# Kernel optimization log

Hardware: AMD Instinct MI355X
Metric: run time of the kernel (lower is better)

Reference implementation:

```python
import jax, jax.numpy as jnp
import numpy as np

GROUP = 32  # hadamard_group_size == MXFP4 block size
FP4_GRID = np.array([0.0, 0.5, 1.0, 1.5, 2.0, 3.0, 4.0, 6.0], dtype=np.float32)  # e2m1 magnitudes
FP4_MID = np.array([0.25, 0.75, 1.25, 1.75, 2.5, 3.5, 5.0], dtype=np.float32)    # RTN midpoints


def _hadamard(n):
    # Sylvester construction, normalized so H is orthonormal (matches hadamard(n)*n**-0.5)
    H = np.array([[1.0]], dtype=np.float64)
    while H.shape[0] < n:
        H = np.block([[H, H], [H, -H]])
    return (H / np.sqrt(n)).astype(np.float32)


def _pseudo_quant_mxfp4(t, H, gs):
    """Hadamard-rotate per group of 32, then MXFP4 (e2m1 + power-of-two block scale)
    quant-dequant with abs_max scaling and a global scale. STE through the rounding."""
    shp = t.shape
    rot = t.reshape(-1, GROUP) @ H                      # [n_groups, 32] rotated space
    v = jax.lax.stop_gradient(rot) * gs
    absmax = jnp.max(jnp.abs(v), axis=-1, keepdims=True)
    # E8M0 power-of-two shared scale so that absmax/scale <= 6 (max e2m1 value)
    scale = jnp.exp2(jnp.ceil(jnp.log2(absmax / 6.0 + 1e-30)))
    scale = jnp.where(absmax > 0, scale, 1.0)
    u = v / scale
    grid = jnp.asarray(FP4_GRID)
    mid = jnp.asarray(FP4_MID)
    q = jnp.sign(u) * grid[jnp.searchsorted(mid, jnp.abs(u))]  # round-to-nearest e2m1
    dq = q * scale / gs
    out = rot + jax.lax.stop_gradient(dq - rot)         # straight-through estimator
    return out.reshape(shp)


def setup_inputs() -> dict:
    key = jax.random.key(0)
    kx, kw, kb = jax.random.split(key, 3)
    B, S, K, N = 4, 2048, 4096, 4096
    x = jax.random.normal(kx, (B, S, K), jnp.float32)
    weight = jax.random.normal(kw, (N, K), jnp.float32) * (K ** -0.5)
    bias = jax.random.normal(kb, (N,), jnp.float32)
    H = jnp.asarray(_hadamard(GROUP))
    weight_global_scale = jnp.array([3.0], jnp.float32)  # abs_max method
    act_global_scale = jnp.array([3.0], jnp.float32)
    return {"x": x, "weight": weight, "bias": bias, "hadamard_matrix": H,
            "weight_global_scale": weight_global_scale, "act_global_scale": act_global_scale}


def reference(x, weight, bias, hadamard_matrix, weight_global_scale, act_global_scale):
    x_dq = _pseudo_quant_mxfp4(x, hadamard_matrix, act_global_scale[0])
    w_dq = _pseudo_quant_mxfp4(weight, hadamard_matrix, weight_global_scale[0])
    # both operands stay in the rotated space; per-group Hadamard is orthogonal so
    # x_rot @ w_rot^T == x @ w^T up to quantization error (QuTLASS semantics)
    return jnp.einsum('bsk,nk->bsn', x_dq, w_dq) + bias
```

## Files before the change

kernel.cpp:

```cpp
#include <hip/hip_runtime.h>
#include <hip/hip_bf16.h>

typedef int   i32x4  __attribute__((ext_vector_type(4)));
typedef int   i32x8  __attribute__((ext_vector_type(8)));
typedef float f32x16 __attribute__((ext_vector_type(16)));

__device__ inline void gload_lds16(const void* g, void* l) {
  __builtin_amdgcn_global_load_lds((const __attribute__((address_space(1))) void*)g,
                                   (__attribute__((address_space(3))) void*)l, 16, 0, 0);
}
__device__ inline void gload_lds4(const void* g, void* l) {
  __builtin_amdgcn_global_load_lds((const __attribute__((address_space(1))) void*)g,
                                   (__attribute__((address_space(3))) void*)l, 4, 0, 0);
}
__device__ inline i32x8 pad8(i32x4 v) {
  i32x8 r;
  r[0] = v[0]; r[1] = v[1]; r[2] = v[2]; r[3] = v[3];
  r[4] = 0; r[5] = 0; r[6] = 0; r[7] = 0;
  return r;
}

__global__ __launch_bounds__(256) void quant_fused(const float* __restrict__ x,
                                                   const float* __restrict__ wt,
                                                   unsigned char* __restrict__ xq,
                                                   unsigned char* __restrict__ xsc,
                                                   unsigned char* __restrict__ wq,
                                                   unsigned char* __restrict__ wsc,
                                                   const float* __restrict__ ags,
                                                   const float* __restrict__ wgs,
                                                   int xg, int Mrows, int Nrows, int kg) {
  const int first = blockIdx.x * 256;
  const bool isX = first < xg;
  const float* in        = isX ? x   : wt;
  unsigned char* outq    = isX ? xq  : wq;
  unsigned char* outsc   = isX ? xsc : wsc;
  const float gs         = isX ? ags[0] : wgs[0];
  const int rows         = isX ? Mrows : Nrows;
  const int base         = isX ? first : first - xg;
  const int g = base + threadIdx.x;
  const int r = g / kg, j = g - r * kg;

  float t[32];
  const float4* p4 = (const float4*)(in + (size_t)g * 32);
#pragma unroll
  for (int i = 0; i < 8; ++i) {
    float4 v4 = p4[i];
    t[4 * i + 0] = v4.x; t[4 * i + 1] = v4.y;
    t[4 * i + 2] = v4.z; t[4 * i + 3] = v4.w;
  }
#pragma unroll
  for (int s = 0; s < 5; ++s) {
    const int hh = 1 << s;
#pragma unroll
    for (int i = 0; i < 32; ++i) {
      if ((i & hh) == 0) {
        float a = t[i], b = t[i + hh];
        t[i] = a + b;
        t[i + hh] = a - b;
      }
    }
  }

  const float c = 0.17677669529663687f;
  float v[32];
  float am = 0.0f;
#pragma unroll
  for (int i = 0; i < 32; ++i) {
    float vi = (t[i] * c) * gs;
    v[i] = vi;
    am = fmaxf(am, fabsf(vi));
  }

  float a6 = am / 6.0f;
  int ex;
  float mant = frexpf(a6, &ex);
  int e = (mant == 0.5f) ? ex - 1 : ex;
  if (e < -127) e = -127;
  if (e > 127) e = 127;
  float inv_s = ldexpf(1.0f, -e);

  unsigned int dw[4] = {0u, 0u, 0u, 0u};
#pragma unroll
  for (int i = 0; i < 32; ++i) {
    float u = v[i] * inv_s;
    float au = fabsf(u);
    int idx = (au > 0.25f) + (au > 0.75f) + (au > 1.25f) + (au > 1.75f)
            + (au > 2.5f) + (au > 3.5f) + (au > 5.0f);
    int code = idx | ((u < 0.0f) ? 8 : 0);
    dw[i >> 3] |= (unsigned)code << ((i & 7) * 4);
  }
  i32x4 packed;
  packed[0] = (int)dw[0]; packed[1] = (int)dw[1];
  packed[2] = (int)dw[2]; packed[3] = (int)dw[3];
  *(i32x4*)(outq + (size_t)r * ((size_t)kg * 16) + (size_t)j * 16) = packed;

  int s = j >> 3, j0 = j & 7;
  int p = ((j0 & 1) << 2) | (j0 >> 1);
  if (kg == 128) {
    __shared__ unsigned char sl[256];
    sl[(s << 4) | ((r & 1) << 3) | p] = (unsigned char)(e + 127);
    __syncthreads();
    if (threadIdx.x < 64) {
      int si = threadIdx.x >> 2, wd = threadIdx.x & 3;
      unsigned int vv = *(const unsigned int*)&sl[(si << 4) | (wd << 2)];
      size_t r0 = (size_t)(base / 128);
      *(unsigned int*)(outsc + ((size_t)si * rows + r0) * 8 + (wd << 2)) = vv;
    }
  } else {
    outsc[((size_t)s * rows + r) * 8 + p] = (unsigned char)(e + 127);
  }
}


#define STAGE(mb, kt, hh, ldsHalf) do {                                              \
    const unsigned char* _s = (mb) + (size_t)((hh)*64 + (w << 3) + (l >> 3)) * KB2   \
                      + (size_t)(kt) * 128 + (size_t)csw * 16;                       \
    gload_lds16(_s, (unsigned char*)(ldsHalf) + (w << 10));                          \
    gload_lds16(_s + ((size_t)KB2 << 5), (unsigned char*)(ldsHalf) + (w << 10) + 4096); \
  } while (0)

#define STAGE_ASC(kt, bf) gload_lds4(AscG + ((size_t)(kt) * M + brow) * 8 + (tid << 2), \
                                     (unsigned char*)&asc[bf][0] + (w << 8))
#define STAGE_BSC(kt, bf) gload_lds4(BscG + ((size_t)(kt) * N + bcol) * 8 + (tid << 2), \
                                     (unsigned char*)&bsc[bf][0] + (w << 8))

#define STAGESET(kt, bf) do {                                                        \
    STAGE(Bb, kt, 0, &lds[bf][1][0]); STAGE(Bb, kt, 1, &lds[bf][1][8192]);           \
    STAGE_BSC(kt, bf);                                                               \
    STAGE(Ab, kt, 0, &lds[bf][0][0]); STAGE(Ab, kt, 1, &lds[bf][0][8192]);           \
    STAGE_ASC(kt, bf);                                                               \
  } while (0)

#define LOADB(bf) do {                                                               \
    const unsigned char* _bb = &lds[bf][1][0];                                       \
    _Pragma("unroll")                                                                \
    for (int nt = 0; nt < 2; ++nt) {                                                 \
      int row = wn * 64 + nt * 32 + (l & 31);                                        \
      int xr = row & 7;                                                              \
      _Pragma("unroll")                                                              \
      for (int kk = 0; kk < 4; ++kk)                                                 \
        bfr[nt][kk] = *(const i32x4*)(_bb + row * 128 + (((kk * 2 + h) ^ xr) << 4)); \
      sb[nt] = *(const int*)((const unsigned char*)&bsc[bf][0] + row * 8 + h * 4);   \
    } } while (0)

#define LOADA(bf) do {                                                               \
    const unsigned char* _ab = &lds[bf][0][0];                                       \
    _Pragma("unroll")                                                                \
    for (int mt = 0; mt < 2; ++mt) {                                                 \
      int row = wm * 64 + mt * 32 + (l & 31);                                        \
      int xr = row & 7;                                                              \
      _Pragma("unroll")                                                              \
      for (int kk = 0; kk < 4; ++kk)                                                 \
        af[mt][kk] = *(const i32x4*)(_ab + row * 128 + (((kk * 2 + h) ^ xr) << 4));  \
      sa[mt] = *(const int*)((const unsigned char*)&asc[bf][0] + row * 8 + h * 4);   \
    } } while (0)

#define MF1(mt, nt, kk)                                                              \
  acc[mt][nt] = __builtin_amdgcn_mfma_scale_f32_32x32x64_f8f6f4(                     \
      pad8(af[mt][kk]), pad8(bfr[nt][kk]), acc[mt][nt], 4, 4, kk, sa[mt], kk, sb[nt]);

#define MFMAQ16() do {                                                               \
    __builtin_amdgcn_s_setprio(1);                                                   \
    MF1(0, 0, 0) MF1(0, 1, 0) MF1(1, 0, 0) MF1(1, 1, 0)                              \
    MF1(0, 0, 1) MF1(0, 1, 1) MF1(1, 0, 1) MF1(1, 1, 1)                              \
    MF1(0, 0, 2) MF1(0, 1, 2) MF1(1, 0, 2) MF1(1, 1, 2)                              \
    MF1(0, 0, 3) MF1(0, 1, 3) MF1(1, 0, 3) MF1(1, 1, 3)                              \
    __builtin_amdgcn_s_setprio(0);                                                   \
  } while (0)

#define DRAIN_THEN_BAR() do {                                                        \
    asm volatile("s_waitcnt lgkmcnt(0)" ::: "memory");                               \
    __builtin_amdgcn_sched_barrier(0);                                               \
    __builtin_amdgcn_s_barrier();                                                    \
  } while (0)

#define ENDP() __builtin_amdgcn_s_barrier()
#define VM10() asm volatile("s_waitcnt vmcnt(10)" ::: "memory")

__global__ __launch_bounds__(256, 2) void gemm128_fp4(const unsigned char* __restrict__ Aq,
                                                      const unsigned char* __restrict__ Bq,
                                                      const unsigned char* __restrict__ AscG,
                                                      const unsigned char* __restrict__ BscG,
                                                      float* __restrict__ C,
                                                      const float* __restrict__ bias,
                                                      const float* __restrict__ gsx,
                                                      const float* __restrict__ gsw,
                                                      int M, int N, int K) {
  __shared__ __align__(16) unsigned char lds[2][2][16384];
  __shared__ __align__(16) unsigned char asc[2][1024];
  __shared__ __align__(16) unsigned char bsc[2][1024];

  const int tid = threadIdx.x;
  const int w = tid >> 6, l = tid & 63;
  const int wm = w >> 1, wn = w & 1;
  const int h = l >> 5;
  const int csw = (l & 7) ^ (l >> 3);
  const int KB2 = K >> 1;

  const int ntn = N >> 7;
  const int nwg = gridDim.x;
  int r_t, c_t;
  {
    int bid = blockIdx.x;
    if ((nwg & 7) == 0) {
      int x = bid & 7, o = bid >> 3, cpx = nwg >> 3;
      int rpx = cpx / ntn;
      if ((ntn & 7) == 0 && rpx > 0 && (cpx % ntn) == 0) {
        int g8 = o & 7, rr = (o >> 3) % rpx, ss = o / (8 * rpx);
        r_t = x * rpx + rr;
        c_t = ss * 8 + g8;
      } else {
        int lin = x * cpx + o;
        r_t = lin / ntn; c_t = lin % ntn;
      }
    } else {
      r_t = bid / ntn; c_t = bid % ntn;
    }
  }
  const size_t brow = (size_t)r_t * 128;
  const size_t bcol = (size_t)c_t * 128;

  const unsigned char* Ab = Aq + brow * (size_t)KB2;
  const unsigned char* Bb = Bq + bcol * (size_t)KB2;

  f32x16 acc[2][2];
#pragma unroll
  for (int m = 0; m < 2; ++m)
#pragma unroll
    for (int n = 0; n < 2; ++n)
#pragma unroll
      for (int r = 0; r < 16; ++r) acc[m][n][r] = 0.0f;

  i32x4 af[2][4], bfr[2][4];
  int sa[2], sb[2];

  const int nkt = K / 256;

  STAGESET(0, 0);
  STAGESET(1, 1);
  VM10();
  __builtin_amdgcn_s_barrier();

  for (int t = 0; t < nkt; ++t) {
    const int p = t & 1;
    const int t2 = (t + 2 < nkt) ? t + 2 : nkt - 1;

    LOADB(p); LOADA(p);
    DRAIN_THEN_BAR();
    STAGESET(t2, p);
    __builtin_amdgcn_sched_barrier(0);
    MFMAQ16();
    VM10();
    ENDP();
  }

  const float inv = 1.0f / (gsx[0] * gsw[0]);
#pragma unroll
  for (int nt = 0; nt < 2; ++nt) {
    const int col = (int)bcol + wn * 64 + nt * 32 + (l & 31);
    const float bv = bias[col];
#pragma unroll
    for (int mt = 0; mt < 2; ++mt) {
      const size_t rbase = brow + (size_t)(wm * 64 + mt * 32 + 4 * h);
#pragma unroll
      for (int r = 0; r < 16; ++r) {
        const size_t row = rbase + (r & 3) + 8 * (r >> 2);
        C[row * (size_t)N + col] = acc[mt][nt][r] * inv + bv;
      }
    }
  }
}

extern "C" void kernel_launch(void* const* d_in, const int* in_sizes, int n_in,
                              void* d_out, int out_size, void* d_ws, size_t ws_size,
                              hipStream_t stream) {
  const float* x    = (const float*)d_in[0];
  const float* wgt  = (const float*)d_in[1];
  const float* bias = (const float*)d_in[2];
  const float* wgs  = (const float*)d_in[4];
  const float* ags  = (const float*)d_in[5];

  const int N = in_sizes[2];
  const int K = in_sizes[1] / N;
  const int M = in_sizes[0] / K;
  const int kg = K / 32;

  unsigned char* aq  = (unsigned char*)d_ws;
  unsigned char* bq  = aq + (size_t)M * (K / 2);
  unsigned char* asc = bq + (size_t)N * (K / 2);
  unsigned char* bsc = asc + (size_t)M * kg;

  const int xg = in_sizes[0] / 32;
  const int wg = in_sizes[1] / 32;
  quant_fused<<<dim3((xg + wg) / 256), dim3(256), 0, stream>>>(
      x, wgt, aq, asc, bq, bsc, ags, wgs, xg, M, N, kg);

  dim3 grid((M / 128) * (N / 128));
  gemm128_fp4<<<grid, dim3(256), 0, stream>>>(aq, bq, asc, bsc, (float*)d_out, bias,
                                              ags, wgs, M, N, K);
}
```

Measured before the change: 148.7 us.

## Split 128x128 FP4 GEMM tile across eight waves instead of four

Doubles the GEMM workgroup to 512 threads, arranged as a 2x4 grid of waves. Each wave now computes a 64x32 sub-tile (two MFMA accumulators instead of four), and the global-to-LDS staging loads are spread across the eight waves. The goal is more waves in flight to hide latency and fewer accumulator registers per wave. In exchange, A fragments are re-read from LDS by more waves, each wave has fewer MFMAs per barrier, and there is more barrier synchronization per unit of work.

```diff
diff --git a/kernel.cpp b/kernel.cpp
--- a/kernel.cpp
+++ b/kernel.cpp
@@ -112,36 +112,32 @@
 }
 
 
-#define STAGE(mb, kt, hh, ldsHalf) do {                                              \
+#define STAGE1(mb, kt, hh, ldsAB) do {                                               \
     const unsigned char* _s = (mb) + (size_t)((hh)*64 + (w << 3) + (l >> 3)) * KB2   \
                       + (size_t)(kt) * 128 + (size_t)csw * 16;                       \
-    gload_lds16(_s, (unsigned char*)(ldsHalf) + (w << 10));                          \
-    gload_lds16(_s + ((size_t)KB2 << 5), (unsigned char*)(ldsHalf) + (w << 10) + 4096); \
-  } while (0)
-
-#define STAGE_ASC(kt, bf) gload_lds4(AscG + ((size_t)(kt) * M + brow) * 8 + (tid << 2), \
-                                     (unsigned char*)&asc[bf][0] + (w << 8))
-#define STAGE_BSC(kt, bf) gload_lds4(BscG + ((size_t)(kt) * N + bcol) * 8 + (tid << 2), \
-                                     (unsigned char*)&bsc[bf][0] + (w << 8))
+    gload_lds16(_s, (unsigned char*)(ldsAB) + (hh) * 8192 + (w << 10));              \
+  } while (0)
 
 #define STAGESET(kt, bf) do {                                                        \
-    STAGE(Bb, kt, 0, &lds[bf][1][0]); STAGE(Bb, kt, 1, &lds[bf][1][8192]);           \
-    STAGE_BSC(kt, bf);                                                               \
-    STAGE(Ab, kt, 0, &lds[bf][0][0]); STAGE(Ab, kt, 1, &lds[bf][0][8192]);           \
-    STAGE_ASC(kt, bf);                                                               \
+    STAGE1(Bb, kt, 0, &lds[bf][1][0]); STAGE1(Bb, kt, 1, &lds[bf][1][0]);            \
+    STAGE1(Ab, kt, 0, &lds[bf][0][0]); STAGE1(Ab, kt, 1, &lds[bf][0][0]);            \
+    if (w < 4)                                                                       \
+      gload_lds4(AscG + ((size_t)(kt) * M + brow) * 8 + ((tid & 255) << 2),          \
+                 (unsigned char*)&asc[bf][0] + ((w & 3) << 8));                      \
+    else                                                                             \
+      gload_lds4(BscG + ((size_t)(kt) * N + bcol) * 8 + ((tid & 255) << 2),          \
+                 (unsigned char*)&bsc[bf][0] + ((w & 3) << 8));                      \
   } while (0)
 
 #define LOADB(bf) do {                                                               \
     const unsigned char* _bb = &lds[bf][1][0];                                       \
+    int row = wn * 32 + (l & 31);                                                    \
+    int xr = row & 7;                                                                \
     _Pragma("unroll")                                                                \
-    for (int nt = 0; nt < 2; ++nt) {                                                 \
-      int row = wn * 64 + nt * 32 + (l & 31);                                        \
-      int xr = row & 7;                                                              \
-      _Pragma("unroll")                                                              \
-      for (int kk = 0; kk < 4; ++kk)                                                 \
-        bfr[nt][kk] = *(const i32x4*)(_bb + row * 128 + (((kk * 2 + h) ^ xr) << 4)); \
-      sb[nt] = *(const int*)((const unsigned char*)&bsc[bf][0] + row * 8 + h * 4);   \
-    } } while (0)
+    for (int kk = 0; kk < 4; ++kk)                                                   \
+      bfr[kk] = *(const i32x4*)(_bb + row * 128 + (((kk * 2 + h) ^ xr) << 4));       \
+    sb = *(const int*)((const unsigned char*)&bsc[bf][0] + row * 8 + h * 4);         \
+  } while (0)
 
 #define LOADA(bf) do {                                                               \
     const unsigned char* _ab = &lds[bf][0][0];                                       \
@@ -155,16 +151,14 @@
       sa[mt] = *(const int*)((const unsigned char*)&asc[bf][0] + row * 8 + h * 4);   \
     } } while (0)
 
-#define MF1(mt, nt, kk)                                                              \
-  acc[mt][nt] = __builtin_amdgcn_mfma_scale_f32_32x32x64_f8f6f4(                     \
-      pad8(af[mt][kk]), pad8(bfr[nt][kk]), acc[mt][nt], 4, 4, kk, sa[mt], kk, sb[nt]);
-
-#define MFMAQ16() do {                                                               \
+#define MF1(mt, kk)                                                                  \
+  acc[mt] = __builtin_amdgcn_mfma_scale_f32_32x32x64_f8f6f4(                         \
+      pad8(af[mt][kk]), pad8(bfr[kk]), acc[mt], 4, 4, kk, sa[mt], kk, sb);
+
+#define MFMAQ8() do {                                                                \
     __builtin_amdgcn_s_setprio(1);                                                   \
-    MF1(0, 0, 0) MF1(0, 1, 0) MF1(1, 0, 0) MF1(1, 1, 0)                              \
-    MF1(0, 0, 1) MF1(0, 1, 1) MF1(1, 0, 1) MF1(1, 1, 1)                              \
-    MF1(0, 0, 2) MF1(0, 1, 2) MF1(1, 0, 2) MF1(1, 1, 2)                              \
-    MF1(0, 0, 3) MF1(0, 1, 3) MF1(1, 0, 3) MF1(1, 1, 3)                              \
+    MF1(0, 0) MF1(1, 0) MF1(0, 1) MF1(1, 1)                                          \
+    MF1(0, 2) MF1(1, 2) MF1(0, 3) MF1(1, 3)                                          \
     __builtin_amdgcn_s_setprio(0);                                                   \
   } while (0)
 
@@ -175,9 +169,9 @@
   } while (0)
 
 #define ENDP() __builtin_amdgcn_s_barrier()
-#define VM10() asm volatile("s_waitcnt vmcnt(10)" ::: "memory")
-
-__global__ __launch_bounds__(256, 2) void gemm128_fp4(const unsigned char* __restrict__ Aq,
+#define VM5()  asm volatile("s_waitcnt vmcnt(5)" ::: "memory")
+
+__global__ __launch_bounds__(512, 4) void gemm128_fp4(const unsigned char* __restrict__ Aq,
                                                       const unsigned char* __restrict__ Bq,
                                                       const unsigned char* __restrict__ AscG,
                                                       const unsigned char* __restrict__ BscG,
@@ -192,7 +186,7 @@
 
   const int tid = threadIdx.x;
   const int w = tid >> 6, l = tid & 63;
-  const int wm = w >> 1, wn = w & 1;
+  const int wm = w >> 2, wn = w & 3;
   const int h = l >> 5;
   const int csw = (l & 7) ^ (l >> 3);
   const int KB2 = K >> 1;
@@ -223,22 +217,20 @@
   const unsigned char* Ab = Aq + brow * (size_t)KB2;
   const unsigned char* Bb = Bq + bcol * (size_t)KB2;
 
-  f32x16 acc[2][2];
+  f32x16 acc[2];
 #pragma unroll
   for (int m = 0; m < 2; ++m)
 #pragma unroll
-    for (int n = 0; n < 2; ++n)
-#pragma unroll
-      for (int r = 0; r < 16; ++r) acc[m][n][r] = 0.0f;
-
-  i32x4 af[2][4], bfr[2][4];
-  int sa[2], sb[2];
+    for (int r = 0; r < 16; ++r) acc[m][r] = 0.0f;
+
+  i32x4 af[2][4], bfr[4];
+  int sa[2], sb;
 
   const int nkt = K / 256;
 
   STAGESET(0, 0);
   STAGESET(1, 1);
-  VM10();
+  VM5();
   __builtin_amdgcn_s_barrier();
 
   for (int t = 0; t < nkt; ++t) {
@@ -249,15 +241,14 @@
     DRAIN_THEN_BAR();
     STAGESET(t2, p);
     __builtin_amdgcn_sched_barrier(0);
-    MFMAQ16();
-    VM10();
+    MFMAQ8();
+    VM5();
     ENDP();
   }
 
   const float inv = 1.0f / (gsx[0] * gsw[0]);
-#pragma unroll
-  for (int nt = 0; nt < 2; ++nt) {
-    const int col = (int)bcol + wn * 64 + nt * 32 + (l & 31);
+  {
+    const int col = (int)bcol + wn * 32 + (l & 31);
     const float bv = bias[col];
 #pragma unroll
     for (int mt = 0; mt < 2; ++mt) {
@@ -265,7 +256,7 @@
 #pragma unroll
       for (int r = 0; r < 16; ++r) {
         const size_t row = rbase + (r & 3) + 8 * (r >> 2);
-        C[row * (size_t)N + col] = acc[mt][nt][r] * inv + bv;
+        C[row * (size_t)N + col] = acc[mt][r] * inv + bv;
       }
     }
   }
@@ -296,6 +287,6 @@
       x, wgt, aq, asc, bq, bsc, ags, wgs, xg, M, N, kg);
 
   dim3 grid((M / 128) * (N / 128));
-  gemm128_fp4<<<grid, dim3(256), 0, stream>>>(aq, bq, asc, bsc, (float*)d_out, bias,
+  gemm128_fp4<<<grid, dim3(512), 0, stream>>>(aq, bq, asc, bsc, (float*)d_out, bias,
                                               ags, wgs, M, N, K);
 }
```

New measurement: 155.0 us. 4.2% more time.

## Enlarge FP4 GEMM block tile to 256x256 with 512-thread workgroups

Applied to the files above, without the earlier changes.

Changes the MXFP4 scaled-MFMA GEMM from 128x128 tiles with 4 waves to 256x256 tiles with 8 waves. Each wave now computes a 64x128 sub-tile: 2x4 accumulators and 32 MFMAs per k-step. LDS staging and scale buffers are resized to match, and the grid shrinks to (M/256)*(N/256) blocks. The aim is more operand reuse per byte loaded and less global/L2 traffic. In exchange it uses about 136KB of LDS per block and more registers, so the 2-blocks-per-CU launch bound cannot be met, and the 256-block grid gives at most one block per CU.

```diff
diff --git a/kernel.cpp b/kernel.cpp
--- a/kernel.cpp
+++ b/kernel.cpp
@@ -112,39 +112,41 @@
 }
 
 
-#define STAGE(mb, kt, hh, ldsHalf) do {                                              \
-    const unsigned char* _s = (mb) + (size_t)((hh)*64 + (w << 3) + (l >> 3)) * KB2   \
-                      + (size_t)(kt) * 128 + (size_t)csw * 16;                       \
-    gload_lds16(_s, (unsigned char*)(ldsHalf) + (w << 10));                          \
-    gload_lds16(_s + ((size_t)KB2 << 5), (unsigned char*)(ldsHalf) + (w << 10) + 4096); \
-  } while (0)
-
-#define STAGE_ASC(kt, bf) gload_lds4(AscG + ((size_t)(kt) * M + brow) * 8 + (tid << 2), \
-                                     (unsigned char*)&asc[bf][0] + (w << 8))
-#define STAGE_BSC(kt, bf) gload_lds4(BscG + ((size_t)(kt) * N + bcol) * 8 + (tid << 2), \
-                                     (unsigned char*)&bsc[bf][0] + (w << 8))
+#define STAGE_A(kt, jj, bf) do {                                                     \
+    int _row = (jj) * 64 + w * 8 + (l >> 3);                                         \
+    const unsigned char* _s = Ab + (size_t)_row * KB2 + (size_t)(kt) * 128           \
+                              + (size_t)csw * 16;                                    \
+    gload_lds16(_s, (unsigned char*)&ldsA[bf][0] + ((jj) * 64 + w * 8) * 128);       \
+  } while (0)
+
+#define STAGE_B(kt, jj, bf) do {                                                     \
+    int _row = (jj) * 64 + w * 8 + (l >> 3);                                         \
+    const unsigned char* _s = Bb + (size_t)_row * KB2 + (size_t)(kt) * 128           \
+                              + (size_t)csw * 16;                                    \
+    gload_lds16(_s, (unsigned char*)&ldsB[bf][0] + ((jj) * 64 + w * 8) * 128);       \
+  } while (0)
 
 #define STAGESET(kt, bf) do {                                                        \
-    STAGE(Bb, kt, 0, &lds[bf][1][0]); STAGE(Bb, kt, 1, &lds[bf][1][8192]);           \
-    STAGE_BSC(kt, bf);                                                               \
-    STAGE(Ab, kt, 0, &lds[bf][0][0]); STAGE(Ab, kt, 1, &lds[bf][0][8192]);           \
-    STAGE_ASC(kt, bf);                                                               \
-  } while (0)
-
-#define LOADB(bf) do {                                                               \
-    const unsigned char* _bb = &lds[bf][1][0];                                       \
+    STAGE_B(kt, 0, bf); STAGE_B(kt, 1, bf); STAGE_B(kt, 2, bf); STAGE_B(kt, 3, bf);  \
+    gload_lds4(BscG + ((size_t)(kt) * N + bcol) * 8 + (tid << 2),                    \
+               (unsigned char*)&bsc[bf][0] + (w << 8));                              \
+    STAGE_A(kt, 0, bf); STAGE_A(kt, 1, bf); STAGE_A(kt, 2, bf); STAGE_A(kt, 3, bf);  \
+    gload_lds4(AscG + ((size_t)(kt) * M + brow) * 8 + (tid << 2),                    \
+               (unsigned char*)&asc[bf][0] + (w << 8));                              \
+  } while (0)
+
+#define READFRAGS(bf) do {                                                           \
+    const unsigned char* _bb = &ldsB[bf][0];                                         \
     _Pragma("unroll")                                                                \
-    for (int nt = 0; nt < 2; ++nt) {                                                 \
-      int row = wn * 64 + nt * 32 + (l & 31);                                        \
+    for (int nt = 0; nt < 4; ++nt) {                                                 \
+      int row = wn * 128 + nt * 32 + (l & 31);                                       \
       int xr = row & 7;                                                              \
       _Pragma("unroll")                                                              \
       for (int kk = 0; kk < 4; ++kk)                                                 \
         bfr[nt][kk] = *(const i32x4*)(_bb + row * 128 + (((kk * 2 + h) ^ xr) << 4)); \
       sb[nt] = *(const int*)((const unsigned char*)&bsc[bf][0] + row * 8 + h * 4);   \
-    } } while (0)
-
-#define LOADA(bf) do {                                                               \
-    const unsigned char* _ab = &lds[bf][0][0];                                       \
+    }                                                                                \
+    const unsigned char* _ab = &ldsA[bf][0];                                         \
     _Pragma("unroll")                                                                \
     for (int mt = 0; mt < 2; ++mt) {                                                 \
       int row = wm * 64 + mt * 32 + (l & 31);                                        \
@@ -159,12 +161,16 @@
   acc[mt][nt] = __builtin_amdgcn_mfma_scale_f32_32x32x64_f8f6f4(                     \
       pad8(af[mt][kk]), pad8(bfr[nt][kk]), acc[mt][nt], 4, 4, kk, sa[mt], kk, sb[nt]);
 
-#define MFMAQ16() do {                                                               \
+#define MFMAQ32() do {                                                               \
     __builtin_amdgcn_s_setprio(1);                                                   \
-    MF1(0, 0, 0) MF1(0, 1, 0) MF1(1, 0, 0) MF1(1, 1, 0)                              \
-    MF1(0, 0, 1) MF1(0, 1, 1) MF1(1, 0, 1) MF1(1, 1, 1)                              \
-    MF1(0, 0, 2) MF1(0, 1, 2) MF1(1, 0, 2) MF1(1, 1, 2)                              \
-    MF1(0, 0, 3) MF1(0, 1, 3) MF1(1, 0, 3) MF1(1, 1, 3)                              \
+    MF1(0, 0, 0) MF1(0, 1, 0) MF1(0, 2, 0) MF1(0, 3, 0)                              \
+    MF1(1, 0, 0) MF1(1, 1, 0) MF1(1, 2, 0) MF1(1, 3, 0)                              \
+    MF1(0, 0, 1) MF1(0, 1, 1) MF1(0, 2, 1) MF1(0, 3, 1)                              \
+    MF1(1, 0, 1) MF1(1, 1, 1) MF1(1, 2, 1) MF1(1, 3, 1)                              \
+    MF1(0, 0, 2) MF1(0, 1, 2) MF1(0, 2, 2) MF1(0, 3, 2)                              \
+    MF1(1, 0, 2) MF1(1, 1, 2) MF1(1, 2, 2) MF1(1, 3, 2)                              \
+    MF1(0, 0, 3) MF1(0, 1, 3) MF1(0, 2, 3) MF1(0, 3, 3)                              \
+    MF1(1, 0, 3) MF1(1, 1, 3) MF1(1, 2, 3) MF1(1, 3, 3)                              \
     __builtin_amdgcn_s_setprio(0);                                                   \
   } while (0)
 
@@ -177,7 +183,7 @@
 #define ENDP() __builtin_amdgcn_s_barrier()
 #define VM10() asm volatile("s_waitcnt vmcnt(10)" ::: "memory")
 
-__global__ __launch_bounds__(256, 2) void gemm128_fp4(const unsigned char* __restrict__ Aq,
+__global__ __launch_bounds__(512, 2) void gemm256_fp4(const unsigned char* __restrict__ Aq,
                                                       const unsigned char* __restrict__ Bq,
                                                       const unsigned char* __restrict__ AscG,
                                                       const unsigned char* __restrict__ BscG,
@@ -186,9 +192,10 @@
                                                       const float* __restrict__ gsx,
                                                       const float* __restrict__ gsw,
                                                       int M, int N, int K) {
-  __shared__ __align__(16) unsigned char lds[2][2][16384];
-  __shared__ __align__(16) unsigned char asc[2][1024];
-  __shared__ __align__(16) unsigned char bsc[2][1024];
+  __shared__ __align__(16) unsigned char ldsA[2][32768];
+  __shared__ __align__(16) unsigned char ldsB[2][32768];
+  __shared__ __align__(16) unsigned char asc[2][2048];
+  __shared__ __align__(16) unsigned char bsc[2][2048];
 
   const int tid = threadIdx.x;
   const int w = tid >> 6, l = tid & 63;
@@ -197,7 +204,7 @@
   const int csw = (l & 7) ^ (l >> 3);
   const int KB2 = K >> 1;
 
-  const int ntn = N >> 7;
+  const int ntn = N >> 8;
   const int nwg = gridDim.x;
   int r_t, c_t;
   {
@@ -217,22 +224,22 @@
       r_t = bid / ntn; c_t = bid % ntn;
     }
   }
-  const size_t brow = (size_t)r_t * 128;
-  const size_t bcol = (size_t)c_t * 128;
+  const size_t brow = (size_t)r_t * 256;
+  const size_t bcol = (size_t)c_t * 256;
 
   const unsigned char* Ab = Aq + brow * (size_t)KB2;
   const unsigned char* Bb = Bq + bcol * (size_t)KB2;
 
-  f32x16 acc[2][2];
+  f32x16 acc[2][4];
 #pragma unroll
   for (int m = 0; m < 2; ++m)
 #pragma unroll
-    for (int n = 0; n < 2; ++n)
+    for (int n = 0; n < 4; ++n)
 #pragma unroll
       for (int r = 0; r < 16; ++r) acc[m][n][r] = 0.0f;
 
-  i32x4 af[2][4], bfr[2][4];
-  int sa[2], sb[2];
+  i32x4 af[2][4], bfr[4][4];
+  int sa[2], sb[4];
 
   const int nkt = K / 256;
 
@@ -245,19 +252,19 @@
     const int p = t & 1;
     const int t2 = (t + 2 < nkt) ? t + 2 : nkt - 1;
 
-    LOADB(p); LOADA(p);
+    READFRAGS(p);
     DRAIN_THEN_BAR();
     STAGESET(t2, p);
     __builtin_amdgcn_sched_barrier(0);
-    MFMAQ16();
+    MFMAQ32();
     VM10();
     ENDP();
   }
 
   const float inv = 1.0f / (gsx[0] * gsw[0]);
 #pragma unroll
-  for (int nt = 0; nt < 2; ++nt) {
-    const int col = (int)bcol + wn * 64 + nt * 32 + (l & 31);
+  for (int nt = 0; nt < 4; ++nt) {
+    const int col = (int)bcol + wn * 128 + nt * 32 + (l & 31);
     const float bv = bias[col];
 #pragma unroll
     for (int mt = 0; mt < 2; ++mt) {
@@ -295,7 +302,7 @@
   quant_fused<<<dim3((xg + wg) / 256), dim3(256), 0, stream>>>(
       x, wgt, aq, asc, bq, bsc, ags, wgs, xg, M, N, kg);
 
-  dim3 grid((M / 128) * (N / 128));
-  gemm128_fp4<<<grid, dim3(256), 0, stream>>>(aq, bq, asc, bsc, (float*)d_out, bias,
+  dim3 grid((M / 256) * (N / 256));
+  gemm256_fp4<<<grid, dim3(512), 0, stream>>>(aq, bq, asc, bsc, (float*)d_out, bias,
                                               ags, wgs, M, N, K);
 }
```

After: 199.7 us. +34.3%, slower.
